# Kernel tuning notes

Hardware: AMD Instinct MI355X
Metric: run time of the kernel (lower is better)

## Reference

```python
import jax, jax.numpy as jnp
import numpy as np

N, IN, OUT, H = 8192, 128, 64, 4
NEG_SLOPE = 0.2   # GATConv leaky-relu slope
EPS = 1e-5        # BatchNorm1d eps
MASK_VAL = -1e9   # masked_fill value for non-edges (finite for grad safety)


def setup_inputs() -> dict:
    key = jax.random.key(0)
    ks = jax.random.split(key, 5)
    x = jax.random.normal(ks[0], (N, IN), jnp.float32)
    adj = jax.random.randint(ks[1], (N, N), 0, 2, jnp.int32)  # dense 0/1 adjacency
    W = jax.random.normal(ks[2], (H, IN, OUT), jnp.float32) * (1.0 / np.sqrt(IN))
    a_i = jax.random.normal(ks[3], (H, OUT), jnp.float32) * (1.0 / np.sqrt(OUT))
    a_j = jax.random.normal(ks[4], (H, OUT), jnp.float32) * (1.0 / np.sqrt(OUT))
    gamma = jnp.ones((H * OUT,), jnp.float32)   # BN weight
    beta = jnp.zeros((H * OUT,), jnp.float32)   # BN bias
    return {"x": x, "adj": adj, "W": W, "a_i": a_i, "a_j": a_j,
            "gamma": gamma, "beta": beta}


def reference(x, adj, W, a_i, a_j, gamma, beta):
    # --- GATConv (dense adjacency, multi-head, concat) ---
    h = jnp.einsum('ni,hio->hno', x, W)              # [H, N, OUT]
    ei = jnp.einsum('hno,ho->hn', h, a_i)            # [H, N] source scores
    ej = jnp.einsum('hno,ho->hn', h, a_j)            # [H, N] target scores
    coe = ei[:, :, None] + ej[:, None, :]            # [H, N, N]
    coe = jnp.where(coe >= 0, coe, NEG_SLOPE * coe)  # leaky_relu
    coe = jnp.where(adj[None, :, :] == 0, MASK_VAL, coe)
    att = jax.nn.softmax(coe, axis=-1)               # segment softmax over neighbors
    out = jnp.einsum('hnm,hmo->hno', att, h)         # weighted aggregation
    out = jnp.transpose(out, (1, 0, 2)).reshape(N, H * OUT)  # concat heads
    # --- BatchNorm1d (training-mode batch stats over nodes) ---
    mean = jnp.mean(out, axis=0)
    var = jnp.var(out, axis=0)
    out = (out - mean) * jax.lax.rsqrt(var + EPS) * gamma + beta
    # --- ReLU ---
    return jax.nn.relu(out)
```

## Files before the change

### kernel.cpp

```cpp
#include <hip/hip_runtime.h>
#include <hip/hip_bf16.h>

#define NN   8192
#define IND  128
#define OUTD 64
#define NH   4
#define NEG_SLOPE 0.2f
#define BN_EPS 1e-5f

typedef __attribute__((ext_vector_type(8))) short bf16x8;
typedef __attribute__((ext_vector_type(4))) float f32x4;
typedef __attribute__((ext_vector_type(4))) int   i32x4;

static __device__ __forceinline__ short f2bf(float f) {
    union { float f; unsigned u; } v; v.f = f;
    return (short)((v.u + 0x8000u) >> 16);
}

__global__ __launch_bounds__(256) void kP_mask(const int* __restrict__ adj,
                                               unsigned int* __restrict__ bm,
                                               float* __restrict__ zreg) {
    int tid = blockIdx.x * 256 + threadIdx.x;
    for (int z = tid; z < 532608; z += 524288)
        ((f32x4*)zreg)[z] = (f32x4){0.f, 0.f, 0.f, 0.f};
    for (int wd = tid; wd < NN * NN / 32; wd += 524288) {
        const int* ap = adj + (size_t)wd * 32;
        unsigned m = 0;
#pragma unroll
        for (int q = 0; q < 8; ++q) {
            i32x4 a = *(const i32x4*)(ap + q * 4);
#pragma unroll
            for (int j = 0; j < 4; ++j)
                m |= (a[j] ? 1u : 0u) << (q * 4 + j);
        }
        bm[wd] = m;
    }
}

__global__ __launch_bounds__(256) void k0_repackW(const float* __restrict__ W,
                                                  short* __restrict__ WB) {
    int tid = blockIdx.x * 256 + threadIdx.x;
    int o = tid & 63, i = (tid >> 6) & 127, h = tid >> 13;
    WB[((h * 16 + (i >> 3)) * 64 + o) * 8 + (i & 7)] = f2bf(W[(h * 128 + i) * 64 + o]);
}

__global__ __launch_bounds__(256) void k1_feat(const float* __restrict__ x,
                                               const short* __restrict__ WB,
                                               const float* __restrict__ a_i,
                                               const float* __restrict__ a_j,
                                               short* __restrict__ hB,
                                               float* __restrict__ t_ei,  float* __restrict__ t_Ri,
                                               float* __restrict__ t_nj,
                                               float* __restrict__ t_E1j, float* __restrict__ t_E2j) {
    int w = threadIdx.x >> 6;
    int l = threadIdx.x & 63;
    int quad = l >> 4, lx = l & 15;
    int rb = blockIdx.x;

    f32x4 acc[4] = {};
#pragma unroll
    for (int ks = 0; ks < 4; ++ks) {
        const float* xp = x + (rb * 16 + lx) * IND + ks * 32 + quad * 8;
        f32x4 xa = *(const f32x4*)xp;
        f32x4 xb = *(const f32x4*)(xp + 4);
        bf16x8 af;
#pragma unroll
        for (int j = 0; j < 4; ++j) { af[j] = f2bf(xa[j]); af[4 + j] = f2bf(xb[j]); }
#pragma unroll
        for (int ot = 0; ot < 4; ++ot) {
            bf16x8 bf = *(const bf16x8*)(WB + ((w * 16 + ks * 4 + quad) * 64 + ot * 16 + lx) * 8);
            acc[ot] = __builtin_amdgcn_mfma_f32_16x16x32_bf16(af, bf, acc[ot], 0, 0, 0);
        }
    }
    float aiv[4], ajv[4];
#pragma unroll
    for (int ot = 0; ot < 4; ++ot) {
        aiv[ot] = a_i[w * 64 + ot * 16 + lx];
        ajv[ot] = a_j[w * 64 + ot * 16 + lx];
    }
#pragma unroll
    for (int reg = 0; reg < 4; ++reg) {
        int row = rb * 16 + quad * 4 + reg;
        float ei = 0.f, ej = 0.f;
#pragma unroll
        for (int ot = 0; ot < 4; ++ot) {
            float hv = acc[ot][reg];
            ei += hv * aiv[ot];
            ej += hv * ajv[ot];
        }
#pragma unroll
        for (int m = 1; m <= 8; m <<= 1) {
            ei += __shfl_xor(ei, m, 64);
            ej += __shfl_xor(ej, m, 64);
        }
        if (lx == reg) {
            t_ei [w * NN + row] = ei;
            t_Ri [w * NN + row] = expf(-0.8f * ei);
            t_nj [w * NN + row] = -ej;
            t_E1j[w * NN + row] = expf(ej);
            t_E2j[w * NN + row] = expf(NEG_SLOPE * ej);
        }
#pragma unroll
        for (int ot = 0; ot < 4; ++ot) {
            int o = ot * 16 + lx;
            hB[((w * 1024 + (row >> 3)) * 64 + o) * 8 + (row & 7)] = f2bf(acc[ot][reg]);
        }
    }
}

__global__ __launch_bounds__(256) void k2_attn(const unsigned char* __restrict__ bmb,
                                               const short* __restrict__ hB,
                                               const float* __restrict__ t_ei,
                                               const float* __restrict__ t_Ri,
                                               const float* __restrict__ t_nj,
                                               const float* __restrict__ t_E1j,
                                               const float* __restrict__ t_E2j,
                                               float* __restrict__ num,
                                               float* __restrict__ Lsum) {
    int w = threadIdx.x >> 6;
    int l = threadIdx.x & 63;
    int quad = l >> 4, lx = l & 15;
    int rb = blockIdx.x >> 2, ks = blockIdx.x & 3;
    int rowbase = rb * 64;
    int tb = w * NN;

    float eiv[4], Riv[4];
    int mbase[4];
#pragma unroll
    for (int r = 0; r < 4; ++r) {
        int i = rowbase + r * 16 + lx;
        eiv[r] = t_ei[tb + i];
        Riv[r] = t_Ri[tb + i];
        mbase[r] = i * 1024 + ks * 256 + quad;
    }

    bf16x8 onesf;
#pragma unroll
    for (int j = 0; j < 8; ++j) onesf[j] = (short)0x3F80;

    f32x4 acc[4][4] = {};
    f32x4 accL[4] = {};
    int k0 = ks * 2048;

    int pm[4];
    f32x4 pnj0, pnj1, pe10, pe11, pe20, pe21;
    {
        int kb = k0 + quad * 8;
        pnj0 = *(const f32x4*)(t_nj  + tb + kb);
        pnj1 = *(const f32x4*)(t_nj  + tb + kb + 4);
        pe10 = *(const f32x4*)(t_E1j + tb + kb);
        pe11 = *(const f32x4*)(t_E1j + tb + kb + 4);
        pe20 = *(const f32x4*)(t_E2j + tb + kb);
        pe21 = *(const f32x4*)(t_E2j + tb + kb + 4);
#pragma unroll
        for (int r = 0; r < 4; ++r) pm[r] = bmb[mbase[r]];
    }

#pragma unroll 1
    for (int kt = 0; kt < 64; ++kt) {
        f32x4 nj0 = pnj0, nj1 = pnj1;
        f32x4 e1j0 = pe10, e1j1 = pe11;
        f32x4 e2j0 = pe20, e2j1 = pe21;
        int mc[4];
#pragma unroll
        for (int r = 0; r < 4; ++r) mc[r] = pm[r];

        int ktn = (kt + 1) & 63;
        int kbn = k0 + ktn * 32 + quad * 8;
        pnj0 = *(const f32x4*)(t_nj  + tb + kbn);
        pnj1 = *(const f32x4*)(t_nj  + tb + kbn + 4);
        pe10 = *(const f32x4*)(t_E1j + tb + kbn);
        pe11 = *(const f32x4*)(t_E1j + tb + kbn + 4);
        pe20 = *(const f32x4*)(t_E2j + tb + kbn);
        pe21 = *(const f32x4*)(t_E2j + tb + kbn + 4);
#pragma unroll
        for (int r = 0; r < 4; ++r) pm[r] = bmb[mbase[r] + ktn * 4];

        int kb = k0 + kt * 32 + quad * 8;
        bf16x8 bfrag[4];
#pragma unroll
        for (int ot = 0; ot < 4; ++ot)
            bfrag[ot] = *(const bf16x8*)(hB + ((w * 1024 + (kb >> 3)) * 64 + ot * 16 + lx) * 8);

        bf16x8 afr[4];
#pragma unroll
        for (int r = 0; r < 4; ++r) {
            union { i32x4 i; bf16x8 b; } af;
#pragma unroll
            for (int jj = 0; jj < 4; ++jj) {
                int j0 = 2 * jj, j1 = 2 * jj + 1;
                float njA = (j0 < 4) ? nj0[j0] : nj1[j0 - 4];
                float njB = (j1 < 4) ? nj0[j1] : nj1[j1 - 4];
                float e1A = (j0 < 4) ? e1j0[j0] : e1j1[j0 - 4];
                float e1B = (j1 < 4) ? e1j0[j1] : e1j1[j1 - 4];
                float e2A = (j0 < 4) ? e2j0[j0] : e2j1[j0 - 4];
                float e2B = (j1 < 4) ? e2j0[j1] : e2j1[j1 - 4];
                float p0 = (eiv[r] >= njA) ? e1A : Riv[r] * e2A;
                float p1 = (eiv[r] >= njB) ? e1B : Riv[r] * e2B;
                p0 = (mc[r] & (1 << j0)) ? p0 : 0.0f;
                p1 = (mc[r] & (1 << j1)) ? p1 : 0.0f;
                af.i[jj] = (int)__builtin_amdgcn_perm(__float_as_uint(p1),
                                                      __float_as_uint(p0),
                                                      0x07060302);
            }
            afr[r] = af.b;
        }
#pragma unroll
        for (int r = 0; r < 4; ++r)
            accL[r] = __builtin_amdgcn_mfma_f32_16x16x32_bf16(afr[r], onesf, accL[r], 0, 0, 0);
#pragma unroll
        for (int r = 0; r < 4; ++r)
#pragma unroll
            for (int ot = 0; ot < 4; ++ot)
                acc[r][ot] = __builtin_amdgcn_mfma_f32_16x16x32_bf16(afr[r], bfrag[ot], acc[r][ot], 0, 0, 0);
    }

#pragma unroll
    for (int r = 0; r < 4; ++r)
        if (lx == 0)
#pragma unroll
            for (int reg = 0; reg < 4; ++reg)
                atomicAdd(&Lsum[w * NN + rowbase + r * 16 + quad * 4 + reg], accL[r][reg]);
#pragma unroll
    for (int r = 0; r < 4; ++r)
#pragma unroll
        for (int ot = 0; ot < 4; ++ot)
#pragma unroll
            for (int reg = 0; reg < 4; ++reg) {
                int row = rowbase + r * 16 + quad * 4 + reg;
                atomicAdd(&num[row * 256 + w * 64 + ot * 16 + lx], acc[r][ot][reg]);
            }
}

__global__ __launch_bounds__(256) void k3_combine(float* __restrict__ num,
                                                  const float* __restrict__ Lsum,
                                                  float* __restrict__ stats) {
    int c = threadIdx.x;
    int h = c >> 6;
    float s = 0.f, s2 = 0.f;
#pragma unroll
    for (int rr = 0; rr < 8; ++rr) {
        int row = blockIdx.x * 8 + rr;
        float L = Lsum[h * NN + row];
        float val = num[row * 256 + c] / L;
        num[row * 256 + c] = val;
        s += val; s2 += val * val;
    }
    atomicAdd(&stats[c], s);
    atomicAdd(&stats[c + 256], s2);
}

__global__ __launch_bounds__(256) void k5_apply(const float* __restrict__ preout,
                                                const float* __restrict__ stats,
                                                const float* __restrict__ gamma,
                                                const float* __restrict__ beta,
                                                float* __restrict__ out) {
    __shared__ float sbnp[512];
    int c = threadIdx.x;
    float mean = stats[c] * (1.0f / NN);
    float var  = stats[c + 256] * (1.0f / NN) - mean * mean;
    float sc = gamma[c] * rsqrtf(var + BN_EPS);
    sbnp[c] = sc;
    sbnp[c + 256] = beta[c] - mean * sc;
    __syncthreads();

    int g = blockIdx.x * 256 + threadIdx.x;
    f32x4 v = *(const f32x4*)(preout + (size_t)g * 4);
    int cb = (g * 4) & 255;
    f32x4 r;
#pragma unroll
    for (int j = 0; j < 4; ++j)
        r[j] = fmaxf(v[j] * sbnp[cb + j] + sbnp[256 + cb + j], 0.0f);
    *(f32x4*)(out + (size_t)g * 4) = r;
}

extern "C" void kernel_launch(void* const* d_in, const int* in_sizes, int n_in,
                              void* d_out, int out_size, void* d_ws, size_t ws_size,
                              hipStream_t stream) {
    (void)in_sizes; (void)n_in; (void)out_size; (void)ws_size;
    const float* x     = (const float*)d_in[0];
    const int*   adj   = (const int*)d_in[1];
    const float* W     = (const float*)d_in[2];
    const float* a_i   = (const float*)d_in[3];
    const float* a_j   = (const float*)d_in[4];
    const float* gamma = (const float*)d_in[5];
    const float* beta  = (const float*)d_in[6];
    float* out = (float*)d_out;

    char* ws = (char*)d_ws;
    short* WB    = (short*)(ws + 0);
    short* hB    = (short*)(ws + 65536);
    float* t_ei  = (float*)(ws + 4259840);
    float* t_Ri  = t_ei + 32768;
    float* t_nj  = t_ei + 2 * 32768;
    float* t_E1j = t_ei + 3 * 32768;
    float* t_E2j = t_ei + 4 * 32768;
    float* num   = (float*)(ws + 5046272);
    float* Lsum  = (float*)(ws + 13434880);
    float* stats = (float*)(ws + 13565952);
    unsigned int* bm = (unsigned int*)(ws + 13568000);

    kP_mask   <<<dim3(2048), dim3(256), 0, stream>>>(adj, bm, num);
    k0_repackW<<<dim3(128),  dim3(256), 0, stream>>>(W, WB);
    k1_feat   <<<dim3(512),  dim3(256), 0, stream>>>(x, WB, a_i, a_j, hB,
                                                     t_ei, t_Ri, t_nj, t_E1j, t_E2j);
    k2_attn   <<<dim3(512),  dim3(256), 0, stream>>>((const unsigned char*)bm, hB,
                                                     t_ei, t_Ri, t_nj, t_E1j, t_E2j,
                                                     num, Lsum);
    k3_combine<<<dim3(1024), dim3(256), 0, stream>>>(num, Lsum, stats);
    k5_apply  <<<dim3(2048), dim3(256), 0, stream>>>(num, stats, gamma, beta, out);
}
```

Baseline: 534.7 us.

## Fuse adjacency bitmask packing into attention kernel via shared memory

Result: faster. 489.1 us (-8.5%).

```diff
diff --git a/kernel.cpp b/kernel.cpp
--- a/kernel.cpp
+++ b/kernel.cpp
@@ -15,26 +15,6 @@
 static __device__ __forceinline__ short f2bf(float f) {
     union { float f; unsigned u; } v; v.f = f;
     return (short)((v.u + 0x8000u) >> 16);
-}
-
-__global__ __launch_bounds__(256) void kP_mask(const int* __restrict__ adj,
-                                               unsigned int* __restrict__ bm,
-                                               float* __restrict__ zreg) {
-    int tid = blockIdx.x * 256 + threadIdx.x;
-    for (int z = tid; z < 532608; z += 524288)
-        ((f32x4*)zreg)[z] = (f32x4){0.f, 0.f, 0.f, 0.f};
-    for (int wd = tid; wd < NN * NN / 32; wd += 524288) {
-        const int* ap = adj + (size_t)wd * 32;
-        unsigned m = 0;
-#pragma unroll
-        for (int q = 0; q < 8; ++q) {
-            i32x4 a = *(const i32x4*)(ap + q * 4);
-#pragma unroll
-            for (int j = 0; j < 4; ++j)
-                m |= (a[j] ? 1u : 0u) << (q * 4 + j);
-        }
-        bm[wd] = m;
-    }
 }
 
 __global__ __launch_bounds__(256) void k0_repackW(const float* __restrict__ W,
@@ -108,7 +88,7 @@
     }
 }
 
-__global__ __launch_bounds__(256) void k2_attn(const unsigned char* __restrict__ bmb,
+__global__ __launch_bounds__(256) void k2_attn(const int* __restrict__ adj,
                                                const short* __restrict__ hB,
                                                const float* __restrict__ t_ei,
                                                const float* __restrict__ t_Ri,
@@ -117,21 +97,42 @@
                                                const float* __restrict__ t_E2j,
                                                float* __restrict__ num,
                                                float* __restrict__ Lsum) {
-    int w = threadIdx.x >> 6;
-    int l = threadIdx.x & 63;
+    __shared__ unsigned char smask[64 * 260];
+    int tid = threadIdx.x;
+    int w = tid >> 6;
+    int l = tid & 63;
     int quad = l >> 4, lx = l & 15;
     int rb = blockIdx.x >> 2, ks = blockIdx.x & 3;
     int rowbase = rb * 64;
     int tb = w * NN;
+    int k0 = ks * 2048;
+
+    {
+        int kc = tid * 8;
+#pragma unroll 2
+        for (int i = 0; i < 64; ++i) {
+            const int* ap = adj + (size_t)(rowbase + i) * NN + k0 + kc;
+            i32x4 a0 = *(const i32x4*)ap;
+            i32x4 a1 = *(const i32x4*)(ap + 4);
+            unsigned m = 0;
+#pragma unroll
+            for (int j = 0; j < 4; ++j) {
+                m |= (a0[j] ? 1u : 0u) << j;
+                m |= (a1[j] ? 1u : 0u) << (4 + j);
+            }
+            smask[i * 260 + tid] = (unsigned char)m;
+        }
+    }
+    __syncthreads();
 
     float eiv[4], Riv[4];
-    int mbase[4];
+    int mrow[4];
 #pragma unroll
     for (int r = 0; r < 4; ++r) {
         int i = rowbase + r * 16 + lx;
         eiv[r] = t_ei[tb + i];
         Riv[r] = t_Ri[tb + i];
-        mbase[r] = i * 1024 + ks * 256 + quad;
+        mrow[r] = (r * 16 + lx) * 260 + quad;
     }
 
     bf16x8 onesf;
@@ -140,9 +141,6 @@
 
     f32x4 acc[4][4] = {};
     f32x4 accL[4] = {};
-    int k0 = ks * 2048;
-
-    int pm[4];
     f32x4 pnj0, pnj1, pe10, pe11, pe20, pe21;
     {
         int kb = k0 + quad * 8;
@@ -152,8 +150,6 @@
         pe11 = *(const f32x4*)(t_E1j + tb + kb + 4);
         pe20 = *(const f32x4*)(t_E2j + tb + kb);
         pe21 = *(const f32x4*)(t_E2j + tb + kb + 4);
-#pragma unroll
-        for (int r = 0; r < 4; ++r) pm[r] = bmb[mbase[r]];
     }
 
 #pragma unroll 1
@@ -163,7 +159,7 @@
         f32x4 e2j0 = pe20, e2j1 = pe21;
         int mc[4];
 #pragma unroll
-        for (int r = 0; r < 4; ++r) mc[r] = pm[r];
+        for (int r = 0; r < 4; ++r) mc[r] = smask[mrow[r] + kt * 4];
 
         int ktn = (kt + 1) & 63;
         int kbn = k0 + ktn * 32 + quad * 8;
@@ -173,8 +169,6 @@
         pe11 = *(const f32x4*)(t_E1j + tb + kbn + 4);
         pe20 = *(const f32x4*)(t_E2j + tb + kbn);
         pe21 = *(const f32x4*)(t_E2j + tb + kbn + 4);
-#pragma unroll
-        for (int r = 0; r < 4; ++r) pm[r] = bmb[mbase[r] + ktn * 4];
 
         int kb = k0 + kt * 32 + quad * 8;
         bf16x8 bfrag[4];
@@ -298,13 +292,13 @@
     float* num   = (float*)(ws + 5046272);
     float* Lsum  = (float*)(ws + 13434880);
     float* stats = (float*)(ws + 13565952);
-    unsigned int* bm = (unsigned int*)(ws + 13568000);
-
-    kP_mask   <<<dim3(2048), dim3(256), 0, stream>>>(adj, bm, num);
+
+    hipMemsetAsync(num, 0, 8388608 + 131072 + 2048, stream);
+
     k0_repackW<<<dim3(128),  dim3(256), 0, stream>>>(W, WB);
     k1_feat   <<<dim3(512),  dim3(256), 0, stream>>>(x, WB, a_i, a_j, hB,
                                                      t_ei, t_Ri, t_nj, t_E1j, t_E2j);
-    k2_attn   <<<dim3(512),  dim3(256), 0, stream>>>((const unsigned char*)bm, hB,
+    k2_attn   <<<dim3(512),  dim3(256), 0, stream>>>(adj, hB,
                                                      t_ei, t_Ri, t_nj, t_E1j, t_E2j,
                                                      num, Lsum);
     k3_combine<<<dim3(1024), dim3(256), 0, stream>>>(num, Lsum, stats);
```
